# Kernel optimization log

Measured on AMD Instinct MI355X. Metric: run time of the kernel, lower is better.

Reference implementation:

```python
import jax, jax.numpy as jnp
import numpy as np

N = 40000      # nodes (single ntype 'paper')
E = 250000     # edges per edge type
IN = 1024      # input feature dim
H, D = 4, 64   # heads, per-head dim
HD = H * D     # h_feats = 256
C = 1024       # num_classes


def setup_inputs() -> dict:
    key = jax.random.key(0)
    ks = jax.random.split(key, 32)
    inp = {"x": jax.random.normal(ks[0], (N, IN), jnp.float32)}
    for t in range(3):
        inp[f"src{t}"] = jax.random.randint(ks[1 + t], (E,), 0, N, jnp.int32)
        inp[f"dst{t}"] = jax.random.randint(ks[4 + t], (E,), 0, N, jnp.int32)
    i = 7
    for l, fin in ((0, IN), (1, HD)):
        for t in range(3):
            inp[f"W{l}_{t}"] = jax.random.normal(ks[i], (fin, HD), jnp.float32) * 0.05; i += 1
            inp[f"al{l}_{t}"] = jax.random.normal(ks[i], (H, D), jnp.float32) * 0.05; i += 1
            inp[f"ar{l}_{t}"] = jax.random.normal(ks[i], (H, D), jnp.float32) * 0.05; i += 1
            inp[f"b{l}_{t}"] = jnp.zeros((HD,), jnp.float32)
    inp["Wout"] = jax.random.normal(ks[i], (HD, C), jnp.float32) * 0.05
    inp["bout"] = jnp.zeros((C,), jnp.float32)
    return inp


def gat_conv(h, src, dst, W, al, ar, b):
    # DGL GATConv: shared fc, additive attention, edge softmax over incoming edges.
    f = (h @ W).reshape(N, H, D)                 # [N,H,D] projected feats
    el = (f * al).sum(-1)                        # [N,H]
    er = (f * ar).sum(-1)                        # [N,H]
    e = jax.nn.leaky_relu(el[src] + er[dst], 0.2)  # [E,H] attn logits
    m = jax.ops.segment_max(e, dst, num_segments=N)        # per-dst max
    ex = jnp.exp(e - m[dst])
    s = jax.ops.segment_sum(ex, dst, num_segments=N)
    a = ex / jnp.where(s[dst] > 0, s[dst], 1.0)  # [E,H] edge softmax
    out = jax.ops.segment_sum(a[:, :, None] * f[src], dst, num_segments=N)  # [N,H,D]
    return out + b.reshape(1, H, D)


def reference(x, src0, dst0, src1, dst1, src2, dst2,
              W0_0, al0_0, ar0_0, b0_0, W0_1, al0_1, ar0_1, b0_1, W0_2, al0_2, ar0_2, b0_2,
              W1_0, al1_0, ar1_0, b1_0, W1_1, al1_1, ar1_1, b1_1, W1_2, al1_2, ar1_2, b1_2,
              Wout, bout):
    edges = [(src0, dst0), (src1, dst1), (src2, dst2)]
    layers = [
        [(W0_0, al0_0, ar0_0, b0_0), (W0_1, al0_1, ar0_1, b0_1), (W0_2, al0_2, ar0_2, b0_2)],
        [(W1_0, al1_0, ar1_0, b1_0), (W1_1, al1_1, ar1_1, b1_1), (W1_2, al1_2, ar1_2, b1_2)],
    ]
    h = x
    for l, ps in enumerate(layers):
        # HeteroGraphConv: per-etype GATConv, 'sum' aggregation across etypes
        hh = sum(gat_conv(h, s, d, *p) for (s, d), p in zip(edges, ps))
        h = hh.reshape(N, HD)                    # flatten heads
        if l != len(layers) - 1:
            h = jax.nn.leaky_relu(h, 0.01)       # F.leaky_relu default slope
            # dropout is identity in eval mode
    return h @ Wout + bout                       # [N, C] logits for 'paper'
```

## Files before the change

kernel.cpp:

```cpp
#include <hip/hip_runtime.h>
#include <hip/hip_bf16.h>
#include <math.h>

#define NN 40000
#define EE 250000
#define HH 4
#define DD 64
#define HDIM 256

typedef __attribute__((ext_vector_type(8))) short short8;
typedef __attribute__((ext_vector_type(4))) float floatx4;
typedef __attribute__((ext_vector_type(4))) unsigned short ushortx4;

#define ASYNC16(G, L) __builtin_amdgcn_global_load_lds( \
    (const __attribute__((address_space(1))) void*)(G), \
    (__attribute__((address_space(3))) void*)(L), 16, 0, 0)

__device__ __forceinline__ float b2f(unsigned short u) {
    return __uint_as_float((unsigned)u << 16);
}
__device__ __forceinline__ unsigned short f2bu(float x) {
    __hip_bfloat16 h = __float2bfloat16(x);
    return *(unsigned short*)&h;
}


__global__ void zero_kernel(int* p, int n) {
    int i = blockIdx.x * blockDim.x + threadIdx.x;
    if (i < n) p[i] = 0;
}

__global__ void count3_kernel(const int* __restrict__ d0, const int* __restrict__ d1,
                              const int* __restrict__ d2, int* __restrict__ deg_all, int n) {
    int i = blockIdx.x * blockDim.x + threadIdx.x;
    int t = blockIdx.y;
    const int* dst = t == 0 ? d0 : (t == 1 ? d1 : d2);
    if (i < n) atomicAdd(&deg_all[t * NN + dst[i]], 1);
}

#define SCAN_PER 40
__global__ __launch_bounds__(1024) void scan3_kernel(const int* __restrict__ deg_all,
                                                     int* __restrict__ rowptr_all, int n) {
    const int* deg = deg_all + blockIdx.x * NN;
    int* rowptr = rowptr_all + blockIdx.x * (NN + 1);
    int tid = threadIdx.x;
    int lane = tid & 63, wv = tid >> 6;
    __shared__ int wsum[16];

    int beg = tid * SCAN_PER;
    int vals[SCAN_PER];
    int loc = 0;
#pragma unroll
    for (int j = 0; j < SCAN_PER; j++) {
        int i = beg + j;
        int v = (i < n) ? deg[i] : 0;
        vals[j] = v;
        loc += v;
    }
    int sc = loc;
#pragma unroll
    for (int off = 1; off < 64; off <<= 1) {
        int t2 = __shfl_up(sc, off);
        if (lane >= off) sc += t2;
    }
    if (lane == 63) wsum[wv] = sc;
    __syncthreads();
    if (wv == 0) {
        int w = (lane < 16) ? wsum[lane] : 0;
#pragma unroll
        for (int off = 1; off < 16; off <<= 1) {
            int t2 = __shfl_up(w, off);
            if (lane >= off) w += t2;
        }
        if (lane < 16) wsum[lane] = w;
    }
    __syncthreads();
    int base = (wv > 0 ? wsum[wv - 1] : 0) + (sc - loc);
    int run = base;
#pragma unroll
    for (int j = 0; j < SCAN_PER; j++) {
        int i = beg + j;
        run += vals[j];
        if (i < n) rowptr[i + 1] = run;
    }
    if (tid == 0) rowptr[0] = 0;
}

__global__ void scatter3_kernel(const int* __restrict__ s0, const int* __restrict__ s1,
                                const int* __restrict__ s2, const int* __restrict__ d0,
                                const int* __restrict__ d1, const int* __restrict__ d2,
                                const int* __restrict__ rowptr_all, int* __restrict__ cur_all,
                                int* __restrict__ colsrc_all, int* __restrict__ coldst_all, int n) {
    int i = blockIdx.x * blockDim.x + threadIdx.x;
    int t = blockIdx.y;
    const int* src = t == 0 ? s0 : (t == 1 ? s1 : s2);
    const int* dst = t == 0 ? d0 : (t == 1 ? d1 : d2);
    if (i < n) {
        int d = dst[i];
        int p = rowptr_all[t * (NN + 1) + d] + atomicAdd(&cur_all[t * NN + d], 1);
        colsrc_all[t * EE + p] = src[i];
        coldst_all[t * EE + p] = d;
    }
}


__global__ void f2b_kernel(const float* __restrict__ in, __hip_bfloat16* __restrict__ o, int n4) {
    int i = blockIdx.x * blockDim.x + threadIdx.x;
    if (i < n4) {
        floatx4 v = *(const floatx4*)(in + (size_t)i * 4);
        ushortx4 r;
        r.x = f2bu(v.x); r.y = f2bu(v.y); r.z = f2bu(v.z); r.w = f2bu(v.w);
        *(ushortx4*)((unsigned short*)o + (size_t)i * 4) = r;
    }
}

__global__ void transb_kernel(const float* __restrict__ W, __hip_bfloat16* __restrict__ Wt,
                              int kshift, int Nc, int total) {
    int i = blockIdx.x * blockDim.x + threadIdx.x;
    if (i < total) {
        int K = 1 << kshift;
        int n2 = i >> kshift, k = i & (K - 1);
        Wt[i] = __float2bfloat16(W[(size_t)k * Nc + n2]);
    }
}


template<bool STORE_BF16>
__global__ __launch_bounds__(256) void gemm_mfma(const __hip_bfloat16* __restrict__ A,
                                                 const __hip_bfloat16* __restrict__ Bt,
                                                 const float* __restrict__ bias,
                                                 float* __restrict__ Cf,
                                                 __hip_bfloat16* __restrict__ Cb,
                                                 int M, int N, int K) {
    __shared__ short As[4096];
    __shared__ short Bs[4096];
    int t = threadIdx.x;
    int lane = t & 63;
    int w = t >> 6;
    int m0 = blockIdx.y * 128;
    int n0 = blockIdx.x * 128;
    int wm = (w >> 1) * 64, wn = (w & 1) * 64;

    int c0 = t, c1 = t + 256;
    int row0 = c0 >> 2, row1 = c1 >> 2;
    int kg0 = (c0 & 3) ^ ((row0 >> 1) & 3);
    int kg1 = (c1 & 3) ^ ((row1 >> 1) & 3);
    int am0 = m0 + row0; if (am0 > M - 1) am0 = M - 1;
    int am1 = m0 + row1; if (am1 > M - 1) am1 = M - 1;
    const __hip_bfloat16* Ag0 = A + (size_t)am0 * K + kg0 * 8;
    const __hip_bfloat16* Ag1 = A + (size_t)am1 * K + kg1 * 8;
    const __hip_bfloat16* Bg0 = Bt + (size_t)(n0 + row0) * K + kg0 * 8;
    const __hip_bfloat16* Bg1 = Bt + (size_t)(n0 + row1) * K + kg1 * 8;
    short* lA0 = &As[(t & 192) * 8];
    short* lA1 = &As[(256 + (t & 192)) * 8];
    short* lB0 = &Bs[(t & 192) * 8];
    short* lB1 = &Bs[(256 + (t & 192)) * 8];

    floatx4 acc[4][4];
#pragma unroll
    for (int i = 0; i < 4; i++)
#pragma unroll
        for (int j = 0; j < 4; j++) acc[i][j] = (floatx4){0.f, 0.f, 0.f, 0.f};

    int quad = lane >> 4;
    int lm = lane & 15;

    for (int k0 = 0; k0 < K; k0 += 32) {
        ASYNC16(Ag0 + k0, lA0);
        ASYNC16(Ag1 + k0, lA1);
        ASYNC16(Bg0 + k0, lB0);
        ASYNC16(Bg1 + k0, lB1);
        __syncthreads();

        short8 af[4], bf[4];
#pragma unroll
        for (int i = 0; i < 4; i++) {
            int rm = wm + i * 16 + lm;
            af[i] = *(const short8*)&As[(rm * 4 + (quad ^ ((rm >> 1) & 3))) * 8];
            int rn = wn + i * 16 + lm;
            bf[i] = *(const short8*)&Bs[(rn * 4 + (quad ^ ((rn >> 1) & 3))) * 8];
        }
#pragma unroll
        for (int i = 0; i < 4; i++)
#pragma unroll
            for (int j = 0; j < 4; j++)
                acc[i][j] = __builtin_amdgcn_mfma_f32_16x16x32_bf16(af[i], bf[j], acc[i][j], 0, 0, 0);
        __syncthreads();
    }

    int lr = (lane >> 4) * 4;
#pragma unroll
    for (int i = 0; i < 4; i++) {
#pragma unroll
        for (int j = 0; j < 4; j++) {
            int col = n0 + wn + j * 16 + lm;
            float bv = bias ? bias[col] : 0.0f;
#pragma unroll
            for (int r = 0; r < 4; r++) {
                int row = m0 + wm + i * 16 + lr + r;
                if (row < M) {
                    float v = acc[i][j][r] + bv;
                    if (STORE_BF16) Cb[(size_t)row * N + col] = __float2bfloat16(v);
                    else            Cf[(size_t)row * N + col] = v;
                }
            }
        }
    }
}


__global__ __launch_bounds__(256) void elr3_kernel(const __hip_bfloat16* __restrict__ f,
                                                   const float* __restrict__ al0, const float* __restrict__ al1,
                                                   const float* __restrict__ al2, const float* __restrict__ ar0,
                                                   const float* __restrict__ ar1, const float* __restrict__ ar2,
                                                   float* __restrict__ el, float* __restrict__ er) {
    int n = blockIdx.x;
    int h = threadIdx.x >> 6;
    int d = threadIdx.x & 63;
#pragma unroll
    for (int t = 0; t < 3; t++) {
        const float* al = t == 0 ? al0 : (t == 1 ? al1 : al2);
        const float* ar = t == 0 ? ar0 : (t == 1 ? ar1 : ar2);
        float v = __bfloat162float(f[(size_t)n * 768 + t * 256 + h * DD + d]);
        float vl = v * al[h * DD + d];
        float vr = v * ar[h * DD + d];
#pragma unroll
        for (int off = 32; off; off >>= 1) {
            vl += __shfl_down(vl, off);
            vr += __shfl_down(vr, off);
        }
        if (d == 0) {
            el[n * 12 + t * 4 + h] = vl;
            er[n * 12 + t * 4 + h] = vr;
        }
    }
}


__global__ __launch_bounds__(256) void attn3_kernel(const int* __restrict__ colsrc_all,
                                                    const int* __restrict__ coldst_all,
                                                    const float* __restrict__ el,
                                                    const float* __restrict__ er,
                                                    float* __restrict__ attn_all) {
    int p = blockIdx.x * blockDim.x + threadIdx.x;
    int t = blockIdx.y;
    if (p >= EE) return;
    int src = colsrc_all[t * EE + p];
    int dst = coldst_all[t * EE + p];
    floatx4 l = *(const floatx4*)(el + (size_t)src * 12 + t * 4);
    floatx4 r = *(const floatx4*)(er + (size_t)dst * 12 + t * 4);
    floatx4 o;
#pragma unroll
    for (int j = 0; j < 4; j++) {
        float e = l[j] + r[j];
        e = (e > 0.f) ? e : 0.2f * e;
        o[j] = __expf(e);
    }
    *(floatx4*)(attn_all + ((size_t)t * EE + p) * 4) = o;
}


__global__ __launch_bounds__(256) void aggregate3v2_kernel(const int* __restrict__ rowptr_all,
                                                           const int* __restrict__ colsrc_all,
                                                           const float* __restrict__ attn_all,
                                                           const __hip_bfloat16* __restrict__ f,
                                                           const float* __restrict__ b0,
                                                           const float* __restrict__ b1,
                                                           const float* __restrict__ b2,
                                                           float slope,
                                                           __hip_bfloat16* __restrict__ outb) {
    int wid = threadIdx.x >> 6;
    int lane = threadIdx.x & 63;
    int n = blockIdx.x * 4 + wid;
    int hh = lane >> 4;
    const unsigned short* fbase = (const unsigned short*)f;

    float t0 = 0.f, t1 = 0.f, t2 = 0.f, t3 = 0.f;
#pragma unroll
    for (int t = 0; t < 3; t++) {
        const int* rowptr = rowptr_all + t * (NN + 1);
        const int* colsrc = colsrc_all + t * EE;
        const float* attn = attn_all + (size_t)t * EE * 4;
        const unsigned short* fb = fbase + t * 256 + lane * 4;
        int beg = rowptr[n], end = rowptr[n + 1];
        float s = 0.f, a0 = 0.f, a1 = 0.f, a2 = 0.f, a3 = 0.f;
        int p = beg;
        for (; p + 4 <= end; p += 4) {
            int i0 = colsrc[p], i1 = colsrc[p + 1], i2 = colsrc[p + 2], i3 = colsrc[p + 3];
            float e0 = attn[p * 4 + hh];
            float e1 = attn[p * 4 + 4 + hh];
            float e2 = attn[p * 4 + 8 + hh];
            float e3 = attn[p * 4 + 12 + hh];
            ushortx4 v0 = *(const ushortx4*)(fb + (size_t)i0 * 768);
            ushortx4 v1 = *(const ushortx4*)(fb + (size_t)i1 * 768);
            ushortx4 v2 = *(const ushortx4*)(fb + (size_t)i2 * 768);
            ushortx4 v3 = *(const ushortx4*)(fb + (size_t)i3 * 768);
            s += (e0 + e1) + (e2 + e3);
            a0 = fmaf(e0, b2f(v0.x), a0); a1 = fmaf(e0, b2f(v0.y), a1);
            a2 = fmaf(e0, b2f(v0.z), a2); a3 = fmaf(e0, b2f(v0.w), a3);
            a0 = fmaf(e1, b2f(v1.x), a0); a1 = fmaf(e1, b2f(v1.y), a1);
            a2 = fmaf(e1, b2f(v1.z), a2); a3 = fmaf(e1, b2f(v1.w), a3);
            a0 = fmaf(e2, b2f(v2.x), a0); a1 = fmaf(e2, b2f(v2.y), a1);
            a2 = fmaf(e2, b2f(v2.z), a2); a3 = fmaf(e2, b2f(v2.w), a3);
            a0 = fmaf(e3, b2f(v3.x), a0); a1 = fmaf(e3, b2f(v3.y), a1);
            a2 = fmaf(e3, b2f(v3.z), a2); a3 = fmaf(e3, b2f(v3.w), a3);
        }
        for (; p < end; p++) {
            int i0 = colsrc[p];
            float e0 = attn[p * 4 + hh];
            ushortx4 v0 = *(const ushortx4*)(fb + (size_t)i0 * 768);
            s += e0;
            a0 = fmaf(e0, b2f(v0.x), a0); a1 = fmaf(e0, b2f(v0.y), a1);
            a2 = fmaf(e0, b2f(v0.z), a2); a3 = fmaf(e0, b2f(v0.w), a3);
        }
        const float* bias = t == 0 ? b0 : (t == 1 ? b1 : b2);
        floatx4 bv = *(const floatx4*)(bias + lane * 4);
        if (s > 0.f) {
            float inv = 1.0f / s;
            t0 += a0 * inv; t1 += a1 * inv; t2 += a2 * inv; t3 += a3 * inv;
        }
        t0 += bv.x; t1 += bv.y; t2 += bv.z; t3 += bv.w;
    }
    t0 = (t0 >= 0.f) ? t0 : slope * t0;
    t1 = (t1 >= 0.f) ? t1 : slope * t1;
    t2 = (t2 >= 0.f) ? t2 : slope * t2;
    t3 = (t3 >= 0.f) ? t3 : slope * t3;
    ushortx4 o;
    o.x = f2bu(t0); o.y = f2bu(t1); o.z = f2bu(t2); o.w = f2bu(t3);
    *(ushortx4*)((unsigned short*)outb + (size_t)n * HDIM + lane * 4) = o;
}


extern "C" void kernel_launch(void* const* d_in, const int* in_sizes, int n_in,
                              void* d_out, int out_size, void* d_ws, size_t ws_size,
                              hipStream_t stream) {
    const float* x = (const float*)d_in[0];
    const int* src[3] = {(const int*)d_in[1], (const int*)d_in[3], (const int*)d_in[5]};
    const int* dst[3] = {(const int*)d_in[2], (const int*)d_in[4], (const int*)d_in[6]};
    const float *W[2][3], *AL[2][3], *AR[2][3], *BB[2][3];
    int idx = 7;
    for (int l = 0; l < 2; l++)
        for (int t = 0; t < 3; t++) {
            W[l][t]  = (const float*)d_in[idx++];
            AL[l][t] = (const float*)d_in[idx++];
            AR[l][t] = (const float*)d_in[idx++];
            BB[l][t] = (const float*)d_in[idx++];
        }
    const float* Wout = (const float*)d_in[31];
    const float* bout = (const float*)d_in[32];
    float* out = (float*)d_out;

    char* p = (char*)d_ws;
    __hip_bfloat16* f_all = (__hip_bfloat16*)p; p += (size_t)NN * 768 * 2;
    char* regionA = p;                          p += (size_t)NN * 1024 * 2;
    float* el_all = (float*)p;                  p += (size_t)NN * 12 * 4;
    float* er_all = (float*)p;                  p += (size_t)NN * 12 * 4;
    __hip_bfloat16* Wt0 = (__hip_bfloat16*)p;   p += (size_t)768 * 1024 * 2;
    __hip_bfloat16* Wt1 = (__hip_bfloat16*)p;   p += (size_t)768 * 256 * 2;
    __hip_bfloat16* Wto = (__hip_bfloat16*)p;   p += (size_t)1024 * 256 * 2;
    int* rowptr_all = (int*)p;                  p += (size_t)3 * (NN + 1) * 4;
    int* colsrc_all = (int*)p;                  p += (size_t)3 * EE * 4;
    int* coldst_all = (int*)p;                  p += (size_t)3 * EE * 4;
    int* cursor_all = (int*)p;                  p += (size_t)3 * NN * 4;
    __hip_bfloat16* xb = (__hip_bfloat16*)regionA;
    __hip_bfloat16* hb = (__hip_bfloat16*)regionA;
    float* attn_all = (float*)(regionA + (size_t)32 * 1024 * 1024);

    zero_kernel<<<(3 * NN + 255) / 256, 256, 0, stream>>>(cursor_all, 3 * NN);
    count3_kernel<<<dim3((EE + 255) / 256, 3), 256, 0, stream>>>(dst[0], dst[1], dst[2], cursor_all, EE);
    scan3_kernel<<<3, 1024, 0, stream>>>(cursor_all, rowptr_all, NN);
    zero_kernel<<<(3 * NN + 255) / 256, 256, 0, stream>>>(cursor_all, 3 * NN);
    scatter3_kernel<<<dim3((EE + 255) / 256, 3), 256, 0, stream>>>(src[0], src[1], src[2],
                                                                   dst[0], dst[1], dst[2],
                                                                   rowptr_all, cursor_all,
                                                                   colsrc_all, coldst_all, EE);

    f2b_kernel<<<(NN * 1024 / 4 + 255) / 256, 256, 0, stream>>>(x, xb, NN * 1024 / 4);
    for (int t = 0; t < 3; t++) {
        transb_kernel<<<(1024 * 256 + 255) / 256, 256, 0, stream>>>(W[0][t], Wt0 + (size_t)t * 256 * 1024, 10, 256, 256 * 1024);
        transb_kernel<<<(256 * 256 + 255) / 256, 256, 0, stream>>>(W[1][t], Wt1 + (size_t)t * 256 * 256, 8, 256, 256 * 256);
    }
    transb_kernel<<<(256 * 1024 + 255) / 256, 256, 0, stream>>>(Wout, Wto, 8, 1024, 1024 * 256);

    gemm_mfma<true><<<dim3(6, 313), 256, 0, stream>>>(xb, Wt0, nullptr, nullptr, f_all, NN, 768, 1024);
    elr3_kernel<<<NN, 256, 0, stream>>>(f_all, AL[0][0], AL[0][1], AL[0][2],
                                        AR[0][0], AR[0][1], AR[0][2], el_all, er_all);
    attn3_kernel<<<dim3((EE + 255) / 256, 3), 256, 0, stream>>>(colsrc_all, coldst_all, el_all, er_all, attn_all);
    aggregate3v2_kernel<<<NN / 4, 256, 0, stream>>>(rowptr_all, colsrc_all, attn_all, f_all,
                                                    BB[0][0], BB[0][1], BB[0][2], 0.01f, hb);

    gemm_mfma<true><<<dim3(6, 313), 256, 0, stream>>>(hb, Wt1, nullptr, nullptr, f_all, NN, 768, 256);
    elr3_kernel<<<NN, 256, 0, stream>>>(f_all, AL[1][0], AL[1][1], AL[1][2],
                                        AR[1][0], AR[1][1], AR[1][2], el_all, er_all);
    attn3_kernel<<<dim3((EE + 255) / 256, 3), 256, 0, stream>>>(colsrc_all, coldst_all, el_all, er_all, attn_all);
    aggregate3v2_kernel<<<NN / 4, 256, 0, stream>>>(rowptr_all, colsrc_all, attn_all, f_all,
                                                    BB[1][0], BB[1][1], BB[1][2], 1.0f, hb);

    gemm_mfma<false><<<dim3(8, 313), 256, 0, stream>>>(hb, Wto, bout, out, nullptr, NN, 1024, 256);
}
```

Baseline: 954.1 us.

## Double-buffer GEMM LDS tiles and remap workgroups across XCDs

The MFMA GEMM now uses two LDS buffers so the async global-to-LDS loads for the next K tile are issued before the MFMAs on the current tile run, overlapping memory with compute. It also remaps the linear block id so consecutive tiles land on the same XCD, aiming for better L2 reuse of shared A/B rows. This doubles LDS use per block, which may lower occupancy. The loop keeps a single __syncthreads per iteration, so whether the next tile has finished loading before it is read depends on that barrier alone.

```diff
diff --git a/kernel.cpp b/kernel.cpp
--- a/kernel.cpp
+++ b/kernel.cpp
@@ -132,13 +132,22 @@
                                                  float* __restrict__ Cf,
                                                  __hip_bfloat16* __restrict__ Cb,
                                                  int M, int N, int K) {
-    __shared__ short As[4096];
-    __shared__ short Bs[4096];
+    __shared__ short As[8192];
+    __shared__ short Bs[8192];
     int t = threadIdx.x;
     int lane = t & 63;
     int w = t >> 6;
-    int m0 = blockIdx.y * 128;
-    int n0 = blockIdx.x * 128;
+
+    int nwg = gridDim.x * gridDim.y;
+    int orig = blockIdx.y * gridDim.x + blockIdx.x;
+    int q = nwg >> 3, r = nwg & 7;
+    int xcd = orig & 7, off = orig >> 3;
+    int wgid = (xcd < r ? xcd * (q + 1) : r * (q + 1) + (xcd - r) * q) + off;
+    int bx = wgid % gridDim.x;
+    int by = wgid / gridDim.x;
+
+    int m0 = by * 128;
+    int n0 = bx * 128;
     int wm = (w >> 1) * 64, wn = (w & 1) * 64;
 
     int c0 = t, c1 = t + 256;
@@ -165,20 +174,31 @@
     int quad = lane >> 4;
     int lm = lane & 15;
 
-    for (int k0 = 0; k0 < K; k0 += 32) {
-        ASYNC16(Ag0 + k0, lA0);
-        ASYNC16(Ag1 + k0, lA1);
-        ASYNC16(Bg0 + k0, lB0);
-        ASYNC16(Bg1 + k0, lB1);
-        __syncthreads();
+    int nt = K >> 5;
+    ASYNC16(Ag0, lA0);
+    ASYNC16(Ag1, lA1);
+    ASYNC16(Bg0, lB0);
+    ASYNC16(Bg1, lB1);
+    __syncthreads();
+
+    for (int tt = 0; tt < nt; ++tt) {
+        int cb = (tt & 1) << 12;
+        int nb = cb ^ 4096;
+        if (tt + 1 < nt) {
+            int k0 = (tt + 1) << 5;
+            ASYNC16(Ag0 + k0, lA0 + nb);
+            ASYNC16(Ag1 + k0, lA1 + nb);
+            ASYNC16(Bg0 + k0, lB0 + nb);
+            ASYNC16(Bg1 + k0, lB1 + nb);
+        }
 
         short8 af[4], bf[4];
 #pragma unroll
         for (int i = 0; i < 4; i++) {
             int rm = wm + i * 16 + lm;
-            af[i] = *(const short8*)&As[(rm * 4 + (quad ^ ((rm >> 1) & 3))) * 8];
+            af[i] = *(const short8*)&As[cb + (rm * 4 + (quad ^ ((rm >> 1) & 3))) * 8];
             int rn = wn + i * 16 + lm;
-            bf[i] = *(const short8*)&Bs[(rn * 4 + (quad ^ ((rn >> 1) & 3))) * 8];
+            bf[i] = *(const short8*)&Bs[cb + (rn * 4 + (quad ^ ((rn >> 1) & 3))) * 8];
         }
 #pragma unroll
         for (int i = 0; i < 4; i++)
@@ -196,10 +216,10 @@
             int col = n0 + wn + j * 16 + lm;
             float bv = bias ? bias[col] : 0.0f;
 #pragma unroll
-            for (int r = 0; r < 4; r++) {
-                int row = m0 + wm + i * 16 + lr + r;
+            for (int r2 = 0; r2 < 4; r2++) {
+                int row = m0 + wm + i * 16 + lr + r2;
                 if (row < M) {
-                    float v = acc[i][j][r] + bv;
+                    float v = acc[i][j][r2] + bv;
                     if (STORE_BF16) Cb[(size_t)row * N + col] = __float2bfloat16(v);
                     else            Cf[(size_t)row * N + col] = v;
                 }
```

Result: faster. 932.4 us (-2.3%).
